# Optimization experiments

Hardware: AMD Instinct MI355X
Metric: run time of the kernel (lower is better)

Reference implementation:

```python
import jax, jax.numpy as jnp
import numpy as np

D_MODEL = 2048
N_HEADS = 16
N_KV_HEADS = 4
HEAD_DIM = 128
ROPE_THETA = 10000.0


def _rope_cos_sin(T, hd, theta):
    # [T, hd//2]
    inv_freq = 1.0 / (theta ** (jnp.arange(0, hd, 2, dtype=jnp.float32) / hd))
    ang = jnp.arange(T, dtype=jnp.float32)[:, None] * inv_freq[None, :]
    return jnp.cos(ang), jnp.sin(ang)


def _apply_rope(x, cos, sin):
    # x: [B, H, T, hd]; rotate-half (Llama-style) RoPE
    hd = x.shape[-1]
    x1, x2 = x[..., : hd // 2], x[..., hd // 2 :]
    c = cos[None, None, :, :]
    s = sin[None, None, :, :]
    return jnp.concatenate([x1 * c - x2 * s, x2 * c + x1 * s], axis=-1)


def setup_inputs() -> dict:
    key = jax.random.key(0)
    ks = jax.random.split(key, 5)
    B, T = 2, 2048
    x = jax.random.normal(ks[0], (B, T, D_MODEL), dtype=jnp.float32)
    sq = 1.0 / np.sqrt(D_MODEL)
    Wq = jax.random.normal(ks[1], (D_MODEL, N_HEADS * HEAD_DIM), dtype=jnp.float32) * sq
    Wk = jax.random.normal(ks[2], (D_MODEL, N_KV_HEADS * HEAD_DIM), dtype=jnp.float32) * sq
    Wv = jax.random.normal(ks[3], (D_MODEL, N_KV_HEADS * HEAD_DIM), dtype=jnp.float32) * sq
    Wo = jax.random.normal(ks[4], (N_HEADS * HEAD_DIM, D_MODEL), dtype=jnp.float32) * sq
    return {"x": x, "Wq": Wq, "Wk": Wk, "Wv": Wv, "Wo": Wo}


def reference(x, Wq, Wk, Wv, Wo):
    B, T, _ = x.shape
    H, KV, hd = N_HEADS, N_KV_HEADS, HEAD_DIM
    n_rep = H // KV

    q = (x @ Wq).reshape(B, T, H, hd).transpose(0, 2, 1, 3)    # [B,H,T,hd]
    k = (x @ Wk).reshape(B, T, KV, hd).transpose(0, 2, 1, 3)   # [B,KV,T,hd]
    v = (x @ Wv).reshape(B, T, KV, hd).transpose(0, 2, 1, 3)

    cos, sin = _rope_cos_sin(T, hd, ROPE_THETA)
    q = _apply_rope(q, cos, sin)
    k = _apply_rope(k, cos, sin)

    # repeat KV heads for GQA: [B,KV,T,hd] -> [B,H,T,hd]
    k = jnp.repeat(k, n_rep, axis=1)
    v = jnp.repeat(v, n_rep, axis=1)

    scale = 1.0 / jnp.sqrt(jnp.float32(hd))
    scores = jnp.einsum("bhqd,bhkd->bhqk", q, k) * scale       # [B,H,T,T]
    causal = jnp.tril(jnp.ones((T, T), dtype=bool))
    scores = jnp.where(causal[None, None, :, :], scores, -jnp.inf)
    attn = jax.nn.softmax(scores, axis=-1)
    out = jnp.einsum("bhqk,bhkd->bhqd", attn, v)               # [B,H,T,hd]
    out = out.transpose(0, 2, 1, 3).reshape(B, T, H * hd)
    return out @ Wo
```

## Files before the change

kernel.cpp:

```cpp
#include <hip/hip_runtime.h>
#include <stdint.h>

#define T_SEQ 2048
#define DM    2048
#define NH    16
#define NKV   4
#define HD    128
#define MROWS 4096
#define NQKV  3072

typedef unsigned short u16;
typedef __bf16 bf16x8 __attribute__((ext_vector_type(8)));
typedef float  f32x4  __attribute__((ext_vector_type(4)));

__device__ __forceinline__ u16 f2b(float f) {
  union { float f; unsigned u; } v; v.f = f;
  return (u16)((v.u + 0x7fffu + ((v.u >> 16) & 1u)) >> 16);
}
__device__ __forceinline__ float b2f(u16 u) {
  union { unsigned u; float f; } v; v.u = ((unsigned)u) << 16;
  return v.f;
}
__device__ __forceinline__ void gl_lds16(const u16* g, u16* l) {
  __builtin_amdgcn_global_load_lds(
      (__attribute__((address_space(1))) void*)g,
      (__attribute__((address_space(3))) void*)l, 16, 0, 0);
}
__device__ __forceinline__ void storev(float* p, float v) { *p = v; }
__device__ __forceinline__ void storev(u16* p, float v)   { *p = f2b(v); }

__global__ __launch_bounds__(256) void k_cvt_x(const float* __restrict__ x,
                                               u16* __restrict__ o, int n) {
  int i = (blockIdx.x * 256 + threadIdx.x) * 4;
  if (i >= n) return;
  float4 v = *(const float4*)(x + i);
  ushort4 r;
  r.x = f2b(v.x); r.y = f2b(v.y); r.z = f2b(v.z); r.w = f2b(v.w);
  *(ushort4*)(o + i) = r;
}

__global__ __launch_bounds__(256) void k_tw4(const float* __restrict__ Wq,
                                             const float* __restrict__ Wk,
                                             const float* __restrict__ Wv,
                                             const float* __restrict__ Wo,
                                             u16* __restrict__ WT,
                                             u16* __restrict__ Wot) {
  __shared__ float tl[32][33];
  int z = blockIdx.z;
  const float* in; u16* out; int Nd, xt;
  if (z < 64)      { in = Wq; out = WT;               Nd = 2048; xt = z; }
  else if (z < 80) { in = Wk; out = WT + 2048 * 2048; Nd = 512;  xt = z - 64; }
  else if (z < 96) { in = Wv; out = WT + 2560 * 2048; Nd = 512;  xt = z - 80; }
  else             { in = Wo; out = Wot;              Nd = 2048; xt = z - 96; }
  int n0 = xt * 32, k0 = blockIdx.y * 32;
  int tx = threadIdx.x, ty = threadIdx.y;
#pragma unroll
  for (int i = 0; i < 32; i += 8)
    tl[ty + i][tx] = in[(long)(k0 + ty + i) * Nd + n0 + tx];
  __syncthreads();
#pragma unroll
  for (int i = 0; i < 32; i += 8)
    out[(long)(n0 + ty + i) * 2048 + k0 + tx] = f2b(tl[tx][ty + i]);
}

template <int BN, typename OutT>
__global__ __launch_bounds__(512, 2) void k_gemm8(const u16* __restrict__ A,
                                                  const u16* __restrict__ Bt,
                                                  OutT* __restrict__ C,
                                                  int M, int N, int K) {
  constexpr int NJ = BN / 128;
  __shared__ __align__(16) u16 As[2][256 * 64];
  __shared__ __align__(16) u16 Bs[2][BN * 64];
  const int tid = threadIdx.x;
  const int wv = tid >> 6, lane = tid & 63;
  const int quad = lane >> 4, ln = lane & 15;
  const int wm = wv & 1, wn = wv >> 1;
  const long m0 = (long)blockIdx.x * 256;
  const long n0 = (long)blockIdx.y * BN;
  const int so = wv << 1;
  const int lr8 = lane >> 3;
  const int gch = (lane & 7) ^ lr8;

  f32x4 acc[8][2 * NJ] = {};
  bf16x8 Af[4][2], Bf[2 * NJ][2];

  auto stage = [&](const u16* __restrict__ G, long grow0, long kcol, u16* lds) {
#pragma unroll
    for (int o = 0; o < 2; ++o) {
      int lr = (so + o) * 8;
      gl_lds16(G + (grow0 + lr + lr8) * (long)K + kcol + gch * 8, lds + lr * 64);
    }
  };

#define READ_A(MH)                                                            \
  _Pragma("unroll") for (int i = 0; i < 4; ++i)                               \
      _Pragma("unroll") for (int s = 0; s < 2; ++s)                           \
          Af[i][s] = *(const bf16x8*)&asc[((MH)*64 + i * 16 + ln) * 64 +      \
                                          (((s * 4 + quad) ^ (ln & 7)) << 3)];
#define READ_B(NHq)                                                           \
  _Pragma("unroll") for (int jj = 0; jj < NJ; ++jj)                           \
      _Pragma("unroll") for (int s = 0; s < 2; ++s)                           \
          Bf[(NHq)*NJ + jj][s] =                                              \
              *(const bf16x8*)&bsc[(((NHq)*NJ + jj) * 16 + ln) * 64 +         \
                                   (((s * 4 + quad) ^ (ln & 7)) << 3)];
#define MMA_Q(MH, NHq)                                                        \
  _Pragma("unroll") for (int i = 0; i < 4; ++i)                               \
      _Pragma("unroll") for (int jj = 0; jj < NJ; ++jj) {                     \
        acc[(MH)*4 + i][(NHq)*NJ + jj] =                                      \
            __builtin_amdgcn_mfma_f32_16x16x32_bf16(                          \
                Af[i][0], Bf[(NHq)*NJ + jj][0],                               \
                acc[(MH)*4 + i][(NHq)*NJ + jj], 0, 0, 0);                     \
        acc[(MH)*4 + i][(NHq)*NJ + jj] =                                      \
            __builtin_amdgcn_mfma_f32_16x16x32_bf16(                          \
                Af[i][1], Bf[(NHq)*NJ + jj][1],                               \
                acc[(MH)*4 + i][(NHq)*NJ + jj], 0, 0, 0);                     \
      }
#define PH_MID()                                                              \
  __builtin_amdgcn_s_barrier();                                               \
  asm volatile("s_waitcnt lgkmcnt(0)" ::: "memory");                          \
  __builtin_amdgcn_s_setprio(1)
#define PH_END()                                                              \
  __builtin_amdgcn_s_setprio(0);                                              \
  __builtin_amdgcn_s_barrier()

  const int NT = K >> 6;
  if constexpr (NJ == 2) {
    stage(Bt, n0, 0, Bs[0]); stage(Bt, n0 + 128, 0, Bs[0] + 128 * 64);
    stage(A,  m0, 0, As[0]); stage(A,  m0 + 128, 0, As[0] + 128 * 64);
    stage(Bt, n0, 64, Bs[1]); stage(Bt, n0 + 128, 64, Bs[1] + 128 * 64);
    stage(A,  m0, 64, As[1]); stage(A,  m0 + 128, 64, As[1] + 128 * 64);
    asm volatile("s_waitcnt vmcnt(8)" ::: "memory");
    __builtin_amdgcn_s_barrier();

    for (int t = 0; t < NT; ++t) {
      const int par = t & 1;
      const u16* asc = As[par] + wm * (128 * 64);
      const u16* bsc = Bs[par] + wn * (32 * NJ * 64);
      u16* sa = As[par];
      u16* sb = Bs[par];
      const bool pf = (t + 2 < NT);
      const long kc2 = (long)(t + 2) * 64;
      READ_A(0); READ_B(0);
      PH_MID(); MMA_Q(0, 0); PH_END();
      READ_B(1);
      PH_MID(); MMA_Q(0, 1); PH_END();
      if (pf) { stage(Bt, n0, kc2, sb); stage(Bt, n0 + 128, kc2, sb + 128 * 64); }
      READ_A(1);
      PH_MID(); MMA_Q(1, 1); PH_END();
      if (pf) { stage(A, m0, kc2, sa); stage(A, m0 + 128, kc2, sa + 128 * 64); }
      if (pf) asm volatile("s_waitcnt vmcnt(8)" ::: "memory");
      else    asm volatile("s_waitcnt vmcnt(0)" ::: "memory");
      PH_MID(); MMA_Q(1, 0); PH_END();
    }
  } else {
    stage(A,  m0, 0, As[0]); stage(A, m0 + 128, 0, As[0] + 128 * 64);
    stage(Bt, n0, 0, Bs[0]);
    stage(Bt, n0, 64, Bs[1]);
    asm volatile("s_waitcnt vmcnt(2)" ::: "memory");
    __builtin_amdgcn_s_barrier();

    for (int t = 0; t < NT; ++t) {
      const int par = t & 1;
      const u16* asc = As[par] + wm * (128 * 64);
      const u16* bsc = Bs[par] + wn * (32 * NJ * 64);
      const bool pa = (t + 1 < NT), pb = (t + 2 < NT);
      if (pa) {
        stage(A, m0,       (long)(t + 1) * 64, As[par ^ 1]);
        stage(A, m0 + 128, (long)(t + 1) * 64, As[par ^ 1] + 128 * 64);
      }
      READ_A(0); READ_B(0); READ_B(1);
      PH_MID(); MMA_Q(0, 0); MMA_Q(0, 1); PH_END();
      if (pb) stage(Bt, n0, (long)(t + 2) * 64, Bs[par]);
      READ_A(1);
      if (pb) asm volatile("s_waitcnt vmcnt(2)" ::: "memory");
      else    asm volatile("s_waitcnt vmcnt(0)" ::: "memory");
      PH_MID(); MMA_Q(1, 0); MMA_Q(1, 1); PH_END();
    }
  }
#undef READ_A
#undef READ_B
#undef MMA_Q
#undef PH_MID
#undef PH_END
#pragma unroll
  for (int i = 0; i < 8; ++i) {
    long row = m0 + wm * 128 + i * 16 + quad * 4;
#pragma unroll
    for (int j = 0; j < 2 * NJ; ++j) {
      long col = n0 + wn * (32 * NJ) + j * 16 + ln;
#pragma unroll
      for (int r = 0; r < 4; ++r)
        storev(&C[(row + r) * N + col], acc[i][j][r]);
    }
  }
}

__global__ __launch_bounds__(256) void k_rope2(const u16* __restrict__ C,
                                               u16* __restrict__ Qo,
                                               u16* __restrict__ Ko) {
  int idx = blockIdx.x * 256 + threadIdx.x;
  int d = idx & 63;
  int t = (idx >> 6) & (T_SEQ - 1);
  int g = idx >> 17;
  int b = (g >= 20) ? 1 : 0;
  int hh = g - b * 20;
  int isQ = hh < 16;
  int head = isQ ? hh : (hh - 16);
  int coloff = isQ ? 0 : 2048;
  float qscale = isQ ? 0.12751745f : 1.0f;
  u16* o = isQ ? Qo : Ko;
  int nh = isQ ? NH : NKV;
  long inb = (long)(b * T_SEQ + t) * NQKV + coloff + head * HD + d;
  float q1 = b2f(C[inb]);
  float q2 = b2f(C[inb + 64]);
  float inv = __expf(-0.14391156f * (float)d);
  float sn, cs;
  __sincosf((float)t * inv, &sn, &cs);
  long ob = (((long)b * nh + head) * T_SEQ + t) * HD + d;
  o[ob]      = f2b((q1 * cs - q2 * sn) * qscale);
  o[ob + 64] = f2b((q2 * cs + q1 * sn) * qscale);
}

__global__ __launch_bounds__(256) void k_vt(const u16* __restrict__ C,
                                            u16* __restrict__ Vt) {
  __shared__ u16 tl[32][33];
  int bkv = blockIdx.z;
  int t0 = blockIdx.x * 32, d0 = blockIdx.y * 32;
  int tx = threadIdx.x, ty = threadIdx.y;
  int b = bkv >> 2, kv = bkv & 3;
#pragma unroll
  for (int i = 0; i < 32; i += 8)
    tl[ty + i][tx] = C[(long)(b * T_SEQ + t0 + ty + i) * NQKV + 2560 + kv * HD + d0 + tx];
  __syncthreads();
#pragma unroll
  for (int i = 0; i < 32; i += 8)
    Vt[((long)bkv * HD + d0 + ty + i) * T_SEQ + t0 + tx] = tl[tx][ty + i];
}

template <bool DIAG>
__device__ __forceinline__ void p_emit(f32x4 (&S)[4], u16* __restrict__ Pb,
                                       int quad, int ln, int mrow) {
#pragma unroll
  for (int nt = 0; nt < 4; ++nt)
#pragma unroll
    for (int r = 0; r < 4; ++r) {
      float v = S[nt][r];
      if (DIAG) v = (nt * 16 + ln <= mrow + r) ? v : -1e30f;
      float pv = exp2f(v - 8.0f);
      int row = quad * 4 + r;
      int chnk = (nt * 2 + (ln >> 3)) ^ (row & 7);
      *(__bf16*)&Pb[row * 64 + chnk * 8 + (ln & 7)] = (__bf16)pv;
    }
}

__global__ __launch_bounds__(256, 2) void k_attn(const u16* __restrict__ Q,
                                                 const u16* __restrict__ Kg,
                                                 const u16* __restrict__ Vt,
                                                 u16* __restrict__ Og) {
  __shared__ __align__(16) u16 Ks[2][64 * 128];
  __shared__ __align__(16) u16 Vs[2][128 * 64];
  __shared__ __align__(16) u16 Ps[4][2][16 * 64];
  const int tid = threadIdx.x;
  const int wv = tid >> 6, lane = tid & 63;
  const int quad = lane >> 4, ln = lane & 15;
  const int bh = blockIdx.y;
  const int b = bh >> 4, h = bh & 15;
  const int kvh = h >> 2;
  const int p = blockIdx.x;
  const int thi = 31 - p, tlo = p;
  const int qhi = thi * 64 + wv * 16;
  const int qlo = tlo * 64 + wv * 16;

  bf16x8 qfh[4], qfl[4];
  {
    const u16* qp = Q + ((long)bh * T_SEQ + qhi + ln) * HD + quad * 8;
#pragma unroll
    for (int s = 0; s < 4; ++s) qfh[s] = *(const bf16x8*)(qp + s * 32);
    qp = Q + ((long)bh * T_SEQ + qlo + ln) * HD + quad * 8;
#pragma unroll
    for (int s = 0; s < 4; ++s) qfl[s] = *(const bf16x8*)(qp + s * 32);
  }
  bf16x8 onesb;
#pragma unroll
  for (int i = 0; i < 8; ++i) onesb[i] = (__bf16)1.0f;

  f32x4 lh = {0.f, 0.f, 0.f, 0.f}, ll = {0.f, 0.f, 0.f, 0.f};
  f32x4 oh[8] = {}, ol[8] = {};

  const u16* Kb = Kg + (long)(b * NKV + kvh) * T_SEQ * HD;
  const u16* Vb = Vt + (long)(b * NKV + kvh) * HD * T_SEQ;

  auto stageKV = [&](int kt, int idx) {
    const int k0 = kt * 64;
#pragma unroll
    for (int r = 0; r < 4; ++r) {
      int s = r * 256 + tid;
      gl_lds16(Kb + (long)(k0 + (s >> 4)) * HD + (((s & 15) ^ ((s >> 4) & 15)) << 3),
               &Ks[idx][(r * 256 + wv * 64) * 8]);
      gl_lds16(Vb + (long)(s >> 3) * T_SEQ + k0 + (((s & 7) ^ ((s >> 3) & 7)) << 3),
               &Vs[idx][(r * 256 + wv * 64) * 8]);
    }
  };

  stageKV(0, 0);
  asm volatile("s_waitcnt vmcnt(0)" ::: "memory");
  __builtin_amdgcn_s_barrier();

  for (int kt = 0; kt <= thi; ++kt) {
    const int cur = kt & 1;
    if (kt < thi) stageKV(kt + 1, cur ^ 1);
    const u16* Ksc = Ks[cur];
    const u16* Vsc = Vs[cur];
    const bool lo_act = (kt <= tlo);
    f32x4 Sh[4], Sl[4];
    __builtin_amdgcn_s_setprio(1);
#pragma unroll
    for (int nt = 0; nt < 4; ++nt) {
      bf16x8 kb[4];
      const u16* kp = &Ksc[(nt * 16 + ln) * 128];
#pragma unroll
      for (int ss = 0; ss < 4; ++ss)
        kb[ss] = *(const bf16x8*)(kp + (((quad + 4 * ss) ^ ln) << 3));
      f32x4 s = {0.f, 0.f, 0.f, 0.f};
#pragma unroll
      for (int ss = 0; ss < 4; ++ss)
        s = __builtin_amdgcn_mfma_f32_16x16x32_bf16(qfh[ss], kb[ss], s, 0, 0, 0);
      Sh[nt] = s;
      if (lo_act) {
        f32x4 t = {0.f, 0.f, 0.f, 0.f};
#pragma unroll
        for (int ss = 0; ss < 4; ++ss)
          t = __builtin_amdgcn_mfma_f32_16x16x32_bf16(qfl[ss], kb[ss], t, 0, 0, 0);
        Sl[nt] = t;
      }
    }
    __builtin_amdgcn_s_setprio(0);
    if (kt == thi) p_emit<true>(Sh, &Ps[wv][0][0], quad, ln, wv * 16 + quad * 4);
    else           p_emit<false>(Sh, &Ps[wv][0][0], quad, ln, 0);
    if (lo_act) {
      if (kt == tlo) p_emit<true>(Sl, &Ps[wv][1][0], quad, ln, wv * 16 + quad * 4);
      else           p_emit<false>(Sl, &Ps[wv][1][0], quad, ln, 0);
    }
    asm volatile("s_waitcnt lgkmcnt(0)" ::: "memory");
    bf16x8 pfh[2], pfl[2];
#pragma unroll
    for (int ss = 0; ss < 2; ++ss)
      pfh[ss] = *(const bf16x8*)&Ps[wv][0][ln * 64 + (((ss * 4 + quad) ^ (ln & 7)) << 3)];
    if (lo_act) {
#pragma unroll
      for (int ss = 0; ss < 2; ++ss)
        pfl[ss] = *(const bf16x8*)&Ps[wv][1][ln * 64 + (((ss * 4 + quad) ^ (ln & 7)) << 3)];
    }
    __builtin_amdgcn_s_setprio(1);
    lh = __builtin_amdgcn_mfma_f32_16x16x32_bf16(pfh[0], onesb, lh, 0, 0, 0);
    lh = __builtin_amdgcn_mfma_f32_16x16x32_bf16(pfh[1], onesb, lh, 0, 0, 0);
    if (lo_act) {
      ll = __builtin_amdgcn_mfma_f32_16x16x32_bf16(pfl[0], onesb, ll, 0, 0, 0);
      ll = __builtin_amdgcn_mfma_f32_16x16x32_bf16(pfl[1], onesb, ll, 0, 0, 0);
    }
#pragma unroll
    for (int dt = 0; dt < 8; ++dt) {
      bf16x8 vb[2];
      const u16* vp = &Vsc[(dt * 16 + ln) * 64];
#pragma unroll
      for (int ss = 0; ss < 2; ++ss)
        vb[ss] = *(const bf16x8*)(vp + (((quad + 4 * ss) ^ (ln & 7)) << 3));
#pragma unroll
      for (int ss = 0; ss < 2; ++ss)
        oh[dt] = __builtin_amdgcn_mfma_f32_16x16x32_bf16(pfh[ss], vb[ss], oh[dt], 0, 0, 0);
      if (lo_act) {
#pragma unroll
        for (int ss = 0; ss < 2; ++ss)
          ol[dt] = __builtin_amdgcn_mfma_f32_16x16x32_bf16(pfl[ss], vb[ss], ol[dt], 0, 0, 0);
      }
    }
    __builtin_amdgcn_s_setprio(0);
    asm volatile("s_waitcnt vmcnt(0)" ::: "memory");
    __builtin_amdgcn_s_barrier();
  }
  float rh[4], rl[4];
#pragma unroll
  for (int r = 0; r < 4; ++r) { rh[r] = 1.f / lh[r]; rl[r] = 1.f / ll[r]; }
#pragma unroll
  for (int dt = 0; dt < 8; ++dt)
#pragma unroll
    for (int r = 0; r < 4; ++r) {
      long rowh = (long)b * T_SEQ + qhi + quad * 4 + r;
      long rowl = (long)b * T_SEQ + qlo + quad * 4 + r;
      Og[rowh * (NH * HD) + h * HD + dt * 16 + ln] = f2b(oh[dt][r] * rh[r]);
      Og[rowl * (NH * HD) + h * HD + dt * 16 + ln] = f2b(ol[dt][r] * rl[r]);
    }
}

extern "C" void kernel_launch(void* const* d_in, const int* in_sizes, int n_in,
                              void* d_out, int out_size, void* d_ws, size_t ws_size,
                              hipStream_t stream) {
  const float* x  = (const float*)d_in[0];
  const float* Wq = (const float*)d_in[1];
  const float* Wk = (const float*)d_in[2];
  const float* Wv = (const float*)d_in[3];
  const float* Wo = (const float*)d_in[4];
  float* out = (float*)d_out;
  char* ws = (char*)d_ws;
  u16* WT  = (u16*)(ws + 0);
  u16* Wot = (u16*)(ws + 12582912);
  u16* Cq  = (u16*)(ws + 20971520);
  u16* Xb  = (u16*)(ws + 46137344);
  u16* Kb  = (u16*)(ws + 62914560);
  u16* Vtb = (u16*)(ws + 67108864);
  u16* Qb = Xb;
  u16* attn = Cq;

  k_cvt_x<<<8192, 256, 0, stream>>>(x, Xb, MROWS * DM);
  k_tw4<<<dim3(1, 64, 160), dim3(32, 8), 0, stream>>>(Wq, Wk, Wv, Wo, WT, Wot);

  k_gemm8<256, u16><<<dim3(16, 12), 512, 0, stream>>>(Xb, WT, Cq, MROWS, NQKV, DM);

  k_rope2<<<20480, 256, 0, stream>>>(Cq, Qb, Kb);
  k_vt<<<dim3(64, 4, 8), dim3(32, 8), 0, stream>>>(Cq, Vtb);

  k_attn<<<dim3(16, 32), 256, 0, stream>>>(Qb, Kb, Vtb, attn);

  k_gemm8<128, float><<<dim3(16, 16), 512, 0, stream>>>(attn, Wot, out, MROWS, DM, 2048);
}
```

Measured before the change: 310.4 us.

## Unify GEMM main loop with double-buffered fragments and staggered A/B prefetch

Replaces the two NJ-specific GEMM loops with one schedule. It keeps two sets of A and B register fragments, so all four MMA quadrants are computed from fragments read only twice per k-tile instead of re-reading B or A. A is prefetched two tiles ahead and B one tile ahead, with the prefetch issues interleaved between the MMA phases. This cuts LDS read traffic and raises the overlap of loads with MFMA work. In exchange it uses more registers, which could hurt occupancy under launch_bounds(512,2), and the vmcnt/lgkmcnt accounting becomes more fragile.

Result: slower. 325.1 us (+4.7%).

```diff
diff --git a/kernel.cpp b/kernel.cpp
--- a/kernel.cpp
+++ b/kernel.cpp
@@ -82,7 +82,7 @@
   const int gch = (lane & 7) ^ lr8;
 
   f32x4 acc[8][2 * NJ] = {};
-  bf16x8 Af[4][2], Bf[2 * NJ][2];
+  bf16x8 Af0[4][2], Af1[4][2], Bf0[NJ][2], Bf1[NJ][2];
 
   auto stage = [&](const u16* __restrict__ G, long grow0, long kcol, u16* lds) {
 #pragma unroll
@@ -92,28 +92,26 @@
     }
   };
 
-#define READ_A(MH)                                                            \
+#define READ_A_(DST, MH)                                                      \
   _Pragma("unroll") for (int i = 0; i < 4; ++i)                               \
       _Pragma("unroll") for (int s = 0; s < 2; ++s)                           \
-          Af[i][s] = *(const bf16x8*)&asc[((MH)*64 + i * 16 + ln) * 64 +      \
-                                          (((s * 4 + quad) ^ (ln & 7)) << 3)];
-#define READ_B(NHq)                                                           \
+          DST[i][s] = *(const bf16x8*)&asc[((MH)*64 + i * 16 + ln) * 64 +     \
+                                           (((s * 4 + quad) ^ (ln & 7)) << 3)];
+#define READ_B_(DST, NHq)                                                     \
   _Pragma("unroll") for (int jj = 0; jj < NJ; ++jj)                           \
       _Pragma("unroll") for (int s = 0; s < 2; ++s)                           \
-          Bf[(NHq)*NJ + jj][s] =                                              \
+          DST[jj][s] =                                                        \
               *(const bf16x8*)&bsc[(((NHq)*NJ + jj) * 16 + ln) * 64 +         \
                                    (((s * 4 + quad) ^ (ln & 7)) << 3)];
-#define MMA_Q(MH, NHq)                                                        \
+#define MMA_Q_(AF, BF, MH, NHq)                                               \
   _Pragma("unroll") for (int i = 0; i < 4; ++i)                               \
       _Pragma("unroll") for (int jj = 0; jj < NJ; ++jj) {                     \
         acc[(MH)*4 + i][(NHq)*NJ + jj] =                                      \
             __builtin_amdgcn_mfma_f32_16x16x32_bf16(                          \
-                Af[i][0], Bf[(NHq)*NJ + jj][0],                               \
-                acc[(MH)*4 + i][(NHq)*NJ + jj], 0, 0, 0);                     \
+                AF[i][0], BF[jj][0], acc[(MH)*4 + i][(NHq)*NJ + jj], 0, 0, 0);\
         acc[(MH)*4 + i][(NHq)*NJ + jj] =                                      \
             __builtin_amdgcn_mfma_f32_16x16x32_bf16(                          \
-                Af[i][1], Bf[(NHq)*NJ + jj][1],                               \
-                acc[(MH)*4 + i][(NHq)*NJ + jj], 0, 0, 0);                     \
+                AF[i][1], BF[jj][1], acc[(MH)*4 + i][(NHq)*NJ + jj], 0, 0, 0);\
       }
 #define PH_MID()                                                              \
   __builtin_amdgcn_s_barrier();                                               \
@@ -124,62 +122,39 @@
   __builtin_amdgcn_s_barrier()
 
   const int NT = K >> 6;
-  if constexpr (NJ == 2) {
-    stage(Bt, n0, 0, Bs[0]); stage(Bt, n0 + 128, 0, Bs[0] + 128 * 64);
-    stage(A,  m0, 0, As[0]); stage(A,  m0 + 128, 0, As[0] + 128 * 64);
-    stage(Bt, n0, 64, Bs[1]); stage(Bt, n0 + 128, 64, Bs[1] + 128 * 64);
-    stage(A,  m0, 64, As[1]); stage(A,  m0 + 128, 64, As[1] + 128 * 64);
-    asm volatile("s_waitcnt vmcnt(8)" ::: "memory");
-    __builtin_amdgcn_s_barrier();
-
-    for (int t = 0; t < NT; ++t) {
-      const int par = t & 1;
-      const u16* asc = As[par] + wm * (128 * 64);
-      const u16* bsc = Bs[par] + wn * (32 * NJ * 64);
-      u16* sa = As[par];
-      u16* sb = Bs[par];
-      const bool pf = (t + 2 < NT);
-      const long kc2 = (long)(t + 2) * 64;
-      READ_A(0); READ_B(0);
-      PH_MID(); MMA_Q(0, 0); PH_END();
-      READ_B(1);
-      PH_MID(); MMA_Q(0, 1); PH_END();
-      if (pf) { stage(Bt, n0, kc2, sb); stage(Bt, n0 + 128, kc2, sb + 128 * 64); }
-      READ_A(1);
-      PH_MID(); MMA_Q(1, 1); PH_END();
-      if (pf) { stage(A, m0, kc2, sa); stage(A, m0 + 128, kc2, sa + 128 * 64); }
-      if (pf) asm volatile("s_waitcnt vmcnt(8)" ::: "memory");
-      else    asm volatile("s_waitcnt vmcnt(0)" ::: "memory");
-      PH_MID(); MMA_Q(1, 0); PH_END();
-    }
-  } else {
-    stage(A,  m0, 0, As[0]); stage(A, m0 + 128, 0, As[0] + 128 * 64);
-    stage(Bt, n0, 0, Bs[0]);
-    stage(Bt, n0, 64, Bs[1]);
-    asm volatile("s_waitcnt vmcnt(2)" ::: "memory");
-    __builtin_amdgcn_s_barrier();
-
-    for (int t = 0; t < NT; ++t) {
-      const int par = t & 1;
-      const u16* asc = As[par] + wm * (128 * 64);
-      const u16* bsc = Bs[par] + wn * (32 * NJ * 64);
-      const bool pa = (t + 1 < NT), pb = (t + 2 < NT);
-      if (pa) {
-        stage(A, m0,       (long)(t + 1) * 64, As[par ^ 1]);
-        stage(A, m0 + 128, (long)(t + 1) * 64, As[par ^ 1] + 128 * 64);
-      }
-      READ_A(0); READ_B(0); READ_B(1);
-      PH_MID(); MMA_Q(0, 0); MMA_Q(0, 1); PH_END();
-      if (pb) stage(Bt, n0, (long)(t + 2) * 64, Bs[par]);
-      READ_A(1);
-      if (pb) asm volatile("s_waitcnt vmcnt(2)" ::: "memory");
-      else    asm volatile("s_waitcnt vmcnt(0)" ::: "memory");
-      PH_MID(); MMA_Q(1, 0); MMA_Q(1, 1); PH_END();
-    }
+  stage(A,  m0,       0, As[0]);
+  stage(A,  m0 + 128, 0, As[0] + 128 * 64);
+  stage(Bt, n0,       0, Bs[0]);
+  if (NJ == 2) stage(Bt, n0 + 128, 0, Bs[0] + 128 * 64);
+  stage(A,  m0,       64, As[1]);
+  stage(A,  m0 + 128, 64, As[1] + 128 * 64);
+  asm volatile("s_waitcnt vmcnt(4)" ::: "memory");
+  __builtin_amdgcn_s_barrier();
+
+  for (int t = 0; t < NT; ++t) {
+    const int par = t & 1;
+    const u16* asc = As[par] + wm * (128 * 64);
+    const u16* bsc = Bs[par] + wn * (32 * NJ * 64);
+    const bool p1 = (t + 1 < NT), p2 = (t + 2 < NT);
+    const long kc1 = (long)(t + 1) * 64, kc2 = (long)(t + 2) * 64;
+    if (p1) stage(Bt, n0, kc1, Bs[par ^ 1]);
+    READ_A_(Af0, 0); READ_B_(Bf0, 0);
+    asm volatile("s_waitcnt lgkmcnt(8)" ::: "memory");
+    PH_MID(); MMA_Q_(Af0, Bf0, 0, 0); PH_END();
+    if (NJ == 2 && p1) stage(Bt, n0 + 128, kc1, Bs[par ^ 1] + 128 * 64);
+    READ_A_(Af1, 1); READ_B_(Bf1, 1);
+    asm volatile("s_waitcnt lgkmcnt(8)" ::: "memory");
+    PH_MID(); MMA_Q_(Af1, Bf1, 1, 1); PH_END();
+    if (p2) stage(A, m0, kc2, As[par]);
+    PH_MID(); MMA_Q_(Af0, Bf1, 0, 1); PH_END();
+    if (p2) stage(A, m0 + 128, kc2, As[par] + 128 * 64);
+    if (p2) asm volatile("s_waitcnt vmcnt(4)" ::: "memory");
+    else    asm volatile("s_waitcnt vmcnt(0)" ::: "memory");
+    PH_MID(); MMA_Q_(Af1, Bf0, 1, 0); PH_END();
   }
-#undef READ_A
-#undef READ_B
-#undef MMA_Q
+#undef READ_A_
+#undef READ_B_
+#undef MMA_Q_
 #undef PH_MID
 #undef PH_END
 #pragma unroll
```
